# Kernel optimization log

Hardware: AMD Instinct MI355X
Metric: run time of the kernel (lower is better)

The kernel has to match this reference:

```python
import jax, jax.numpy as jnp
import numpy as np

B, I, NN, D = 4, 128, 127, 128   # batch, n_index, nodes without super node, hidden
N = NN + 1                        # nodes including super node
H, L, FFN = 4, 4, 32              # heads, layers, ffn dim
DK = D // H // 2                  # att_size = 16 per head, per stream
SCALE = DK ** -0.5


def layernorm(x, g, b, eps=1e-5):
    m = jnp.mean(x, -1, keepdims=True)
    v = jnp.mean((x - m) ** 2, -1, keepdims=True)
    return (x - m) * jax.lax.rsqrt(v + eps) * g + b


def mha(x, bias, ln_g, ln_b, wq, bq, wk, bk, wv, bv):
    # EncoderLayerSimple: pre-LN then MHA with additive bias, no out-proj (enable_out_layer=False)
    y = layernorm(x, ln_g, ln_b)
    Bx, S, _ = y.shape
    q = (y @ wq.T + bq).reshape(Bx, S, H, DK) * SCALE
    k = (y @ wk.T + bk).reshape(Bx, S, H, DK)
    v = (y @ wv.T + bv).reshape(Bx, S, H, DK)
    s = jnp.einsum('bihd,bjhd->bhij', q, k) + bias
    a = jax.nn.softmax(s, axis=-1)
    return jnp.einsum('bhij,bjhd->bihd', a, v).reshape(Bx, S, H * DK)


def setup_inputs():
    ks = jax.random.split(jax.random.key(0), 24)
    f = jnp.float32
    inp = {
        'node_embedded': jax.random.normal(ks[0], (B, I, NN, D), f),
        'heights': jax.random.normal(ks[1], (B, I, NN, D), f),
        'rel_pos_mat': jax.random.randint(ks[2], (B, I, N, N), 0, 192),
        'tree_attn_bias': jax.random.normal(ks[3], (B, I, N, N), f) * 0.1,
        'index_attn_bias': jax.random.normal(ks[4], (B, N, I, I), f) * 0.1,
        'super_node_emb': jax.random.normal(ks[5], (1, D), f) * 0.02,
        'rel_pos_emb': (jax.random.normal(ks[6], (192, H), f) * 0.02).at[0].set(0.0),  # padding_idx=0
        'super_dist': jax.random.normal(ks[7], (1, H), f) * 0.02,
        'attn_out_w': jax.random.normal(ks[8], (D, D), f) * 0.02,
        'attn_out_b': jnp.zeros((D,), f),
        'ffn_ln_g': jnp.ones((D,), f), 'ffn_ln_b': jnp.zeros((D,), f),
        'ffn_w1': jax.random.normal(ks[9], (FFN, D), f) * 0.02,
        'ffn_b1': jnp.zeros((FFN,), f),
        'ffn_w2': jax.random.normal(ks[10], (D, FFN), f) * 0.02,
        'ffn_b2': jnp.zeros((D,), f),
        'final_ln_g': jnp.ones((D,), f), 'final_ln_b': jnp.zeros((D,), f),
    }
    for pre, base in (('enc1', 11), ('enc2', 17)):
        inp[pre + '_ln_g'] = jnp.ones((L, D), f)
        inp[pre + '_ln_b'] = jnp.zeros((L, D), f)
        for j, nm in enumerate(('wq', 'wk', 'wv')):
            inp[pre + '_' + nm] = jax.random.normal(ks[base + j], (L, H * DK, D), f) * 0.02
            inp[pre + '_b' + nm[1]] = jnp.zeros((L, H * DK), f)
    return inp


def reference(node_embedded, heights, rel_pos_mat, tree_attn_bias, index_attn_bias,
              super_node_emb, rel_pos_emb, super_dist, attn_out_w, attn_out_b,
              ffn_ln_g, ffn_ln_b, ffn_w1, ffn_b1, ffn_w2, ffn_b2, final_ln_g, final_ln_b,
              enc1_ln_g, enc1_ln_b, enc1_wq, enc1_bq, enc1_wk, enc1_bk, enc1_wv, enc1_bv,
              enc2_ln_g, enc2_ln_b, enc2_wq, enc2_bq, enc2_wk, enc2_bk, enc2_wv, enc2_bv):
    node = node_embedded + heights
    sup = jnp.broadcast_to(super_node_emb.reshape(1, 1, 1, D), (B, I, 1, D))
    x = jnp.concatenate([sup, node], axis=2)  # [B, I, N, D]
    # tree attention bias: per-head repeat + rel-pos embedding gather + super-node distance
    rel = rel_pos_emb[rel_pos_mat.reshape(B * I, N, N)]            # [BI, N, N, H]
    tab = tree_attn_bias.reshape(B * I, N, N)[:, None] + jnp.transpose(rel, (0, 3, 1, 2))
    t = super_dist.reshape(1, H, 1)
    tab = tab.at[:, :, 1:, 0].add(t)
    tab = tab.at[:, :, 0, :].add(t)                                # [BI, H, N, N]
    iab = index_attn_bias.reshape(B * N, I, I)[:, None]            # [BN, 1, I, I] (broadcast over heads)
    for l in range(L):
        x1 = jnp.transpose(x, (0, 2, 1, 3)).reshape(B * N, I, D)   # index-axis stream
        x2 = x.reshape(B * I, N, D)                                # node-axis stream
        y1 = mha(x1, iab, enc1_ln_g[l], enc1_ln_b[l], enc1_wq[l], enc1_bq[l],
                 enc1_wk[l], enc1_bk[l], enc1_wv[l], enc1_bv[l])
        y2 = mha(x2, tab, enc2_ln_g[l], enc2_ln_b[l], enc2_wq[l], enc2_bq[l],
                 enc2_wk[l], enc2_bk[l], enc2_wv[l], enc2_bv[l])
        y1 = jnp.transpose(y1.reshape(B, N, I, D // 2), (0, 2, 1, 3))
        y2 = y2.reshape(B, I, N, D // 2)
        y = jnp.concatenate([y1, y2], axis=-1) @ attn_out_w.T + attn_out_b
        x = x + y
        z = layernorm(x, ffn_ln_g, ffn_ln_b)
        z = jax.nn.gelu(z @ ffn_w1.T + ffn_b1, approximate=False) @ ffn_w2.T + ffn_b2
        x = x + z
    return layernorm(x, final_ln_g, final_ln_b)
```

## Files before the change

### kernel.cpp

```cpp
#include <hip/hip_runtime.h>
#include <cstdint>
#include <cstddef>


__device__ __forceinline__ int swz (int r, int c){ return c ^ (((r >> 2) & 7) << 2); }
__device__ __forceinline__ int swzA(int r, int c){ return c ^ ((r & 7) << 2); }

__global__ __launch_bounds__(256) void k_build_x(const float4* __restrict__ ne,
    const float4* __restrict__ hts, const float4* __restrict__ sup,
    float4* __restrict__ X){
  int idx = blockIdx.x * 256 + threadIdx.x;
  int d4 = idx & 31;
  int n  = (idx >> 5) & 127;
  int bi = idx >> 12;
  float4 v;
  if (n == 0){
    v = sup[d4];
  } else {
    size_t s = ((size_t)bi * 127 + (n - 1)) * 32 + d4;
    float4 a = ne[s], h = hts[s];
    v.x = a.x + h.x; v.y = a.y + h.y; v.z = a.z + h.z; v.w = a.w + h.w;
  }
  X[idx] = v;
}

struct QkvArgs {
  const float* x;
  const float* ln_g[2]; const float* ln_b[2];
  const float* w[6];  const float* wb[6];
  float* out[6];
};

__global__ __launch_bounds__(256, 3) void k_qkv(QkvArgs A){
  __shared__ float sY[32 * 128];
  __shared__ float sW[64 * 128];
  const int r0  = blockIdx.x * 32;
  const int enc = blockIdx.y;
  const int t   = threadIdx.x;
  {
    const float4* xs = (const float4*)(A.x + (size_t)r0 * 128);
    #pragma unroll
    for (int it = 0; it < 4; ++it){
      int el = it * 256 + t;
      int rr = el >> 5, c4 = (el & 31) * 4;
      *(float4*)&sY[rr * 128 + swzA(rr, c4)] = xs[el];
    }
  }
  __syncthreads();
  const int row = t >> 3, part = t & 7;
  float s1 = 0.f, s2 = 0.f;
  float4 xv[4];
  #pragma unroll
  for (int q = 0; q < 4; ++q){
    int c4 = part * 16 + q * 4;
    xv[q] = *(const float4*)&sY[row * 128 + swzA(row, c4)];
    s1 += xv[q].x + xv[q].y + xv[q].z + xv[q].w;
    s2 += xv[q].x*xv[q].x + xv[q].y*xv[q].y + xv[q].z*xv[q].z + xv[q].w*xv[q].w;
  }
  s1 += __shfl_xor(s1, 1); s2 += __shfl_xor(s2, 1);
  s1 += __shfl_xor(s1, 2); s2 += __shfl_xor(s2, 2);
  s1 += __shfl_xor(s1, 4); s2 += __shfl_xor(s2, 4);
  float mean = s1 * (1.f / 128.f);
  float rstd = rsqrtf(s2 * (1.f / 128.f) - mean * mean + 1e-5f);
  {
    const float* lg = A.ln_g[enc];
    const float* lb = A.ln_b[enc];
    #pragma unroll
    for (int q = 0; q < 4; ++q){
      int cc = part * 16 + q * 4;
      int a  = row * 128 + swzA(row, cc);
      float4 gv = *(const float4*)&lg[cc];
      float4 bv = *(const float4*)&lb[cc];
      float4 y;
      y.x = (xv[q].x - mean) * rstd * gv.x + bv.x;
      y.y = (xv[q].y - mean) * rstd * gv.y + bv.y;
      y.z = (xv[q].z - mean) * rstd * gv.z + bv.z;
      y.w = (xv[q].w - mean) * rstd * gv.w + bv.w;
      *(float4*)&sY[a] = y;
    }
  }
  const int tc = t & 15, tr = t >> 4;
  const int kb_x  = (tc & 7) << 2;
  const int ra0 = tr * 2, ra1 = tr * 2 + 1;
  const int ka_x0 = (ra0 & 7) << 2;
  const int ka_x1 = (ra1 & 7) << 2;
  for (int g3 = 0; g3 < 3; ++g3){
    const int g = enc * 3 + g3;
    __syncthreads();
    {
      const float4* wsrc = (const float4*)A.w[g];
      #pragma unroll
      for (int it = 0; it < 8; ++it){
        int el = it * 256 + t;
        int rr = el >> 5, c4 = (el & 31) * 4;
        *(float4*)&sW[rr * 128 + swz(rr, c4)] = wsrc[el];
      }
    }
    __syncthreads();
    float acc[2][4] = {};
    #pragma unroll
    for (int k = 0; k < 128; k += 4){
      float4 av[2], bv[4];
      av[0] = *(const float4*)&sY[ra0 * 128 + (k ^ ka_x0)];
      av[1] = *(const float4*)&sY[ra1 * 128 + (k ^ ka_x1)];
      int kb = k ^ kb_x;
      #pragma unroll
      for (int q = 0; q < 4; ++q) bv[q] = *(const float4*)&sW[(tc * 4 + q) * 128 + kb];
      #pragma unroll
      for (int i2 = 0; i2 < 2; ++i2)
        #pragma unroll
        for (int j2 = 0; j2 < 4; ++j2){
          acc[i2][j2] += av[i2].x * bv[j2].x;
          acc[i2][j2] += av[i2].y * bv[j2].y;
          acc[i2][j2] += av[i2].z * bv[j2].z;
          acc[i2][j2] += av[i2].w * bv[j2].w;
        }
    }
    const float scale = (g3 == 0) ? 0.25f : 1.0f;
    const float* wb = A.wb[g];
    const float b0 = wb[tc*4], b1 = wb[tc*4+1], b2 = wb[tc*4+2], b3 = wb[tc*4+3];
    float* outp = A.out[g];
    const int h_ = tc >> 2, u_ = (tc & 3) * 4;
    #pragma unroll
    for (int i2 = 0; i2 < 2; ++i2){
      int gr = r0 + tr * 2 + i2;
      size_t off = ((size_t)((gr >> 7) * 4 + h_)) * 2048 + (gr & 127) * 16 + u_;
      float4 o;
      o.x = (acc[i2][0] + b0) * scale;
      o.y = (acc[i2][1] + b1) * scale;
      o.z = (acc[i2][2] + b2) * scale;
      o.w = (acc[i2][3] + b3) * scale;
      *(float4*)&outp[off] = o;
    }
  }
}

__global__ __launch_bounds__(128, 3) void k_attn1(const float* __restrict__ Q,
    const float* __restrict__ K, const float* __restrict__ V,
    const float* __restrict__ iab, float* __restrict__ YC){
  __shared__ float sK[128][20];
  __shared__ float sV[128][20];
  const int seq = blockIdx.x;
  const int h   = blockIdx.y;
  const int i   = threadIdx.x;
  const int b_ = seq >> 7, n_ = seq & 127;
  const size_t rbase = ((size_t)((b_ * 128 + i) * 4 + h)) * 2048 + n_ * 16;
  #pragma unroll
  for (int u = 0; u < 4; ++u){
    *(float4*)&sK[i][u * 4] = *(const float4*)&K[rbase + u * 4];
    *(float4*)&sV[i][u * 4] = *(const float4*)&V[rbase + u * 4];
  }
  float q[16];
  #pragma unroll
  for (int u = 0; u < 4; ++u){
    float4 v = *(const float4*)&Q[rbase + u * 4];
    q[u*4+0] = v.x; q[u*4+1] = v.y; q[u*4+2] = v.z; q[u*4+3] = v.w;
  }
  __syncthreads();
  const float4* brow = (const float4*)(iab + (size_t)seq * 16384 + (size_t)i * 128);
  float s[128];
  #pragma unroll
  for (int j4 = 0; j4 < 32; ++j4){
    float4 bv4 = brow[j4];
    float bb[4] = {bv4.x, bv4.y, bv4.z, bv4.w};
    #pragma unroll
    for (int u = 0; u < 4; ++u){
      int j = j4 * 4 + u;
      float acc = bb[u];
      #pragma unroll
      for (int u4 = 0; u4 < 4; ++u4){
        float4 kv = *(const float4*)&sK[j][u4 * 4];
        acc += q[u4*4+0]*kv.x + q[u4*4+1]*kv.y + q[u4*4+2]*kv.z + q[u4*4+3]*kv.w;
      }
      s[j] = acc;
    }
  }
  float m = -1e30f;
  #pragma unroll
  for (int j = 0; j < 128; ++j) m = fmaxf(m, s[j]);
  float sum = 0.f;
  #pragma unroll
  for (int j = 0; j < 128; ++j){ float ev = __expf(s[j] - m); s[j] = ev; sum += ev; }
  float inv = 1.f / sum;
  float o[16] = {};
  #pragma unroll
  for (int j = 0; j < 128; ++j){
    float p = s[j];
    #pragma unroll
    for (int u4 = 0; u4 < 4; ++u4){
      float4 vv = *(const float4*)&sV[j][u4 * 4];
      o[u4*4+0] += p * vv.x; o[u4*4+1] += p * vv.y;
      o[u4*4+2] += p * vv.z; o[u4*4+3] += p * vv.w;
    }
  }
  size_t off = (((size_t)(b_ * 128 + i)) * 128 + n_) * 128 + h * 16;
  #pragma unroll
  for (int u = 0; u < 4; ++u){
    float4 v;
    v.x = o[u*4+0]*inv; v.y = o[u*4+1]*inv; v.z = o[u*4+2]*inv; v.w = o[u*4+3]*inv;
    *(float4*)&YC[off + u * 4] = v;
  }
}

__global__ __launch_bounds__(128, 3) void k_attn2(const float* __restrict__ Q,
    const float* __restrict__ K, const float* __restrict__ V,
    const float* __restrict__ tree, const int* __restrict__ mat,
    const float* __restrict__ relemb, const float* __restrict__ sdist,
    float* __restrict__ YC){
  __shared__ float sK[128][20];
  __shared__ float sV[128][20];
  __shared__ float srel[768];
  const int seq = blockIdx.x;
  const int h   = blockIdx.y;
  const int i   = threadIdx.x;
  const size_t base = ((size_t)(seq * 4 + h)) * 2048;
  #pragma unroll
  for (int u = 0; u < 4; ++u){
    *(float4*)&sK[i][u * 4] = *(const float4*)&K[base + i * 16 + u * 4];
    *(float4*)&sV[i][u * 4] = *(const float4*)&V[base + i * 16 + u * 4];
  }
  float q[16];
  #pragma unroll
  for (int u = 0; u < 4; ++u){
    float4 v = *(const float4*)&Q[base + i * 16 + u * 4];
    q[u*4+0] = v.x; q[u*4+1] = v.y; q[u*4+2] = v.z; q[u*4+3] = v.w;
  }
  #pragma unroll
  for (int u = 0; u < 6; ++u) srel[u * 128 + i] = relemb[u * 128 + i];
  const float tsup = sdist[h];
  __syncthreads();
  const float4* trow = (const float4*)(tree + (size_t)seq * 16384 + (size_t)i * 128);
  const int4*   mrow = (const int4*)(mat + (size_t)seq * 16384 + (size_t)i * 128);
  float s[128];
  #pragma unroll
  for (int j4 = 0; j4 < 32; ++j4){
    float4 tv = trow[j4];
    int4  mv  = mrow[j4];
    float bb[4];
    bb[0] = tv.x + srel[mv.x * 4 + h];
    bb[1] = tv.y + srel[mv.y * 4 + h];
    bb[2] = tv.z + srel[mv.z * 4 + h];
    bb[3] = tv.w + srel[mv.w * 4 + h];
    #pragma unroll
    for (int u = 0; u < 4; ++u){
      int j = j4 * 4 + u;
      float acc = bb[u];
      if (i == 0) acc += tsup;
      else if (j == 0) acc += tsup;
      #pragma unroll
      for (int u4 = 0; u4 < 4; ++u4){
        float4 kv = *(const float4*)&sK[j][u4 * 4];
        acc += q[u4*4+0]*kv.x + q[u4*4+1]*kv.y + q[u4*4+2]*kv.z + q[u4*4+3]*kv.w;
      }
      s[j] = acc;
    }
  }
  float m = -1e30f;
  #pragma unroll
  for (int j = 0; j < 128; ++j) m = fmaxf(m, s[j]);
  float sum = 0.f;
  #pragma unroll
  for (int j = 0; j < 128; ++j){ float ev = __expf(s[j] - m); s[j] = ev; sum += ev; }
  float inv = 1.f / sum;
  float o[16] = {};
  #pragma unroll
  for (int j = 0; j < 128; ++j){
    float p = s[j];
    #pragma unroll
    for (int u4 = 0; u4 < 4; ++u4){
      float4 vv = *(const float4*)&sV[j][u4 * 4];
      o[u4*4+0] += p * vv.x; o[u4*4+1] += p * vv.y;
      o[u4*4+2] += p * vv.z; o[u4*4+3] += p * vv.w;
    }
  }
  size_t off = (((size_t)seq) * 128 + i) * 128 + 64 + h * 16;
  #pragma unroll
  for (int u = 0; u < 4; ++u){
    float4 v;
    v.x = o[u*4+0]*inv; v.y = o[u*4+1]*inv; v.z = o[u*4+2]*inv; v.w = o[u*4+3]*inv;
    *(float4*)&YC[off + u * 4] = v;
  }
}

__global__ __launch_bounds__(256, 2) void k_attn_out(const float* __restrict__ YC,
    const float* __restrict__ W, const float* __restrict__ bias, float* __restrict__ X){
  __shared__ float sA[64 * 128];
  __shared__ float sW[64 * 128];
  const int r0 = blockIdx.x * 64, c0 = blockIdx.y * 64;
  const int t  = threadIdx.x;
  {
    const float4* as   = (const float4*)(YC + (size_t)r0 * 128);
    const float4* wsrc = (const float4*)(W + (size_t)c0 * 128);
    #pragma unroll
    for (int it = 0; it < 8; ++it){
      int e  = it * 256 + t;
      int rr = e >> 5, c4 = (e & 31) * 4;
      int cs = swz(rr, c4);
      *(float4*)&sA[rr * 128 + cs] = as[e];
      *(float4*)&sW[rr * 128 + cs] = wsrc[e];
    }
  }
  __syncthreads();
  const int tc = t & 15, tr = t >> 4;
  float acc[4][4] = {};
  #pragma unroll
  for (int k = 0; k < 128; k += 4){
    float4 av[4], bv[4];
    int ka = k ^ ((tr & 7) << 2);
    int kb = k ^ ((tc & 7) << 2);
    #pragma unroll
    for (int q = 0; q < 4; ++q) av[q] = *(const float4*)&sA[(tr * 4 + q) * 128 + ka];
    #pragma unroll
    for (int q = 0; q < 4; ++q) bv[q] = *(const float4*)&sW[(tc * 4 + q) * 128 + kb];
    #pragma unroll
    for (int i2 = 0; i2 < 4; ++i2)
      #pragma unroll
      for (int j2 = 0; j2 < 4; ++j2){
        acc[i2][j2] += av[i2].x * bv[j2].x;
        acc[i2][j2] += av[i2].y * bv[j2].y;
        acc[i2][j2] += av[i2].z * bv[j2].z;
        acc[i2][j2] += av[i2].w * bv[j2].w;
      }
  }
  const float b0 = bias[c0 + tc*4], b1 = bias[c0 + tc*4 + 1],
              b2 = bias[c0 + tc*4 + 2], b3 = bias[c0 + tc*4 + 3];
  #pragma unroll
  for (int i2 = 0; i2 < 4; ++i2){
    int r = r0 + tr * 4 + i2;
    float4* xp = (float4*)&X[(size_t)r * 128 + c0 + tc * 4];
    float4 xv = *xp;
    xv.x += acc[i2][0] + b0;
    xv.y += acc[i2][1] + b1;
    xv.z += acc[i2][2] + b2;
    xv.w += acc[i2][3] + b3;
    *xp = xv;
  }
}

__global__ __launch_bounds__(256, 2) void k_ffn(float* __restrict__ X,
    const float* __restrict__ lg, const float* __restrict__ lb,
    const float* __restrict__ W1, const float* __restrict__ b1,
    const float* __restrict__ W2, const float* __restrict__ b2){
  __shared__ float sW1[32][132];
  __shared__ float sW2[128][36];
  __shared__ float sY[16][132];
  __shared__ float sH[16][33];
  const int t  = threadIdx.x;
  const int r0 = blockIdx.x * 16;
  {
    const float4* w1s = (const float4*)W1;
    #pragma unroll
    for (int it = 0; it < 4; ++it){
      int e = it * 256 + t;
      int r = e >> 5, c4 = (e & 31) * 4;
      *(float4*)&sW1[r][c4] = w1s[e];
    }
    const float4* w2s = (const float4*)W2;
    #pragma unroll
    for (int it = 0; it < 4; ++it){
      int e = it * 256 + t;
      int r = e >> 3, c4 = (e & 7) * 4;
      *(float4*)&sW2[r][c4] = w2s[e];
    }
  }
  const int row = t >> 4, p = t & 15;
  const size_t gb = ((size_t)(r0 + row)) * 128;
  float4 xa = *(const float4*)&X[gb + p * 8];
  float4 xb = *(const float4*)&X[gb + p * 8 + 4];
  float s1 = xa.x + xa.y + xa.z + xa.w + xb.x + xb.y + xb.z + xb.w;
  float s2 = xa.x*xa.x + xa.y*xa.y + xa.z*xa.z + xa.w*xa.w
           + xb.x*xb.x + xb.y*xb.y + xb.z*xb.z + xb.w*xb.w;
  #pragma unroll
  for (int msk = 1; msk < 16; msk <<= 1){ s1 += __shfl_xor(s1, msk); s2 += __shfl_xor(s2, msk); }
  float mean = s1 * (1.f / 128.f);
  float rstd = rsqrtf(s2 * (1.f / 128.f) - mean * mean + 1e-5f);
  {
    float4 g0 = *(const float4*)&lg[p * 8], g1 = *(const float4*)&lg[p * 8 + 4];
    float4 c0 = *(const float4*)&lb[p * 8], c1 = *(const float4*)&lb[p * 8 + 4];
    float4 y0, y1;
    y0.x = (xa.x-mean)*rstd*g0.x + c0.x;  y0.y = (xa.y-mean)*rstd*g0.y + c0.y;
    y0.z = (xa.z-mean)*rstd*g0.z + c0.z;  y0.w = (xa.w-mean)*rstd*g0.w + c0.w;
    y1.x = (xb.x-mean)*rstd*g1.x + c1.x;  y1.y = (xb.y-mean)*rstd*g1.y + c1.y;
    y1.z = (xb.z-mean)*rstd*g1.z + c1.z;  y1.w = (xb.w-mean)*rstd*g1.w + c1.w;
    *(float4*)&sY[row][p * 8]     = y0;
    *(float4*)&sY[row][p * 8 + 4] = y1;
  }
  __syncthreads();
  #pragma unroll
  for (int cc = 0; cc < 2; ++cc){
    int c = p + cc * 16;
    float acc = b1[c];
    #pragma unroll
    for (int k = 0; k < 128; ++k) acc += sY[row][k] * sW1[c][k];
    sH[row][c] = 0.5f * acc * (1.0f + erff(acc * 0.70710678118654752f));
  }
  __syncthreads();
  #pragma unroll
  for (int u = 0; u < 8; ++u){
    int c = p + u * 16;
    float acc = b2[c];
    #pragma unroll
    for (int k = 0; k < 32; ++k) acc += sH[row][k] * sW2[c][k];
    X[gb + c] += acc;
  }
}

__global__ __launch_bounds__(256) void k_final(const float* __restrict__ X,
    const float* __restrict__ g, const float* __restrict__ b, float* __restrict__ out){
  const int t = threadIdx.x;
  const int row = blockIdx.x * 64 + (t >> 2), p = t & 3;
  const float* src = X + (size_t)row * 128 + p * 32;
  float4 v[8];
  float s1 = 0.f, s2 = 0.f;
  #pragma unroll
  for (int u = 0; u < 8; ++u){
    v[u] = *(const float4*)&src[u * 4];
    s1 += v[u].x + v[u].y + v[u].z + v[u].w;
    s2 += v[u].x*v[u].x + v[u].y*v[u].y + v[u].z*v[u].z + v[u].w*v[u].w;
  }
  s1 += __shfl_xor(s1, 1); s2 += __shfl_xor(s2, 1);
  s1 += __shfl_xor(s1, 2); s2 += __shfl_xor(s2, 2);
  float mean = s1 * (1.f / 128.f);
  float rstd = rsqrtf(s2 * (1.f / 128.f) - mean * mean + 1e-5f);
  float* dst = out + (size_t)row * 128 + p * 32;
  #pragma unroll
  for (int u = 0; u < 8; ++u){
    int c = p * 32 + u * 4;
    float4 gv = *(const float4*)&g[c];
    float4 bv = *(const float4*)&b[c];
    float4 o;
    o.x = (v[u].x - mean) * rstd * gv.x + bv.x;
    o.y = (v[u].y - mean) * rstd * gv.y + bv.y;
    o.z = (v[u].z - mean) * rstd * gv.z + bv.z;
    o.w = (v[u].w - mean) * rstd * gv.w + bv.w;
    *(float4*)&dst[u * 4] = o;
  }
}

extern "C" void kernel_launch(void* const* d_in, const int* in_sizes, int n_in,
                              void* d_out, int out_size, void* d_ws, size_t ws_size,
                              hipStream_t stream){
  (void)in_sizes; (void)n_in; (void)out_size; (void)ws_size;
  const float* node_embedded   = (const float*)d_in[0];
  const float* heights         = (const float*)d_in[1];
  const int*   rel_pos_mat     = (const int*)d_in[2];
  const float* tree_attn_bias  = (const float*)d_in[3];
  const float* index_attn_bias = (const float*)d_in[4];
  const float* super_node_emb  = (const float*)d_in[5];
  const float* rel_pos_emb     = (const float*)d_in[6];
  const float* super_dist      = (const float*)d_in[7];
  const float* attn_out_w      = (const float*)d_in[8];
  const float* attn_out_b      = (const float*)d_in[9];
  const float* ffn_ln_g        = (const float*)d_in[10];
  const float* ffn_ln_b        = (const float*)d_in[11];
  const float* ffn_w1          = (const float*)d_in[12];
  const float* ffn_b1          = (const float*)d_in[13];
  const float* ffn_w2          = (const float*)d_in[14];
  const float* ffn_b2          = (const float*)d_in[15];
  const float* final_ln_g      = (const float*)d_in[16];
  const float* final_ln_b      = (const float*)d_in[17];
  const float* e1_ln_g = (const float*)d_in[18];
  const float* e1_ln_b = (const float*)d_in[19];
  const float* e1_wq   = (const float*)d_in[20];
  const float* e1_bq   = (const float*)d_in[21];
  const float* e1_wk   = (const float*)d_in[22];
  const float* e1_bk   = (const float*)d_in[23];
  const float* e1_wv   = (const float*)d_in[24];
  const float* e1_bv   = (const float*)d_in[25];
  const float* e2_ln_g = (const float*)d_in[26];
  const float* e2_ln_b = (const float*)d_in[27];
  const float* e2_wq   = (const float*)d_in[28];
  const float* e2_bq   = (const float*)d_in[29];
  const float* e2_wk   = (const float*)d_in[30];
  const float* e2_bk   = (const float*)d_in[31];
  const float* e2_wv   = (const float*)d_in[32];
  const float* e2_bv   = (const float*)d_in[33];

  float* ws = (float*)d_ws;
  const size_t SZX = 8388608, SZH = 4194304;
  float* X  = ws;
  float* Q1 = X  + SZX;
  float* K1 = Q1 + SZH;
  float* V1 = K1 + SZH;
  float* Q2 = V1 + SZH;
  float* K2 = Q2 + SZH;
  float* V2 = K2 + SZH;
  float* YC = V2 + SZH;

  k_build_x<<<8192, 256, 0, stream>>>((const float4*)node_embedded, (const float4*)heights,
                                      (const float4*)super_node_emb, (float4*)X);
  for (int l = 0; l < 4; ++l){
    QkvArgs A;
    A.x = X;
    A.ln_g[0] = e1_ln_g + l * 128;  A.ln_b[0] = e1_ln_b + l * 128;
    A.ln_g[1] = e2_ln_g + l * 128;  A.ln_b[1] = e2_ln_b + l * 128;
    A.w[0] = e1_wq + (size_t)l * 8192;  A.wb[0] = e1_bq + l * 64;
    A.w[1] = e1_wk + (size_t)l * 8192;  A.wb[1] = e1_bk + l * 64;
    A.w[2] = e1_wv + (size_t)l * 8192;  A.wb[2] = e1_bv + l * 64;
    A.w[3] = e2_wq + (size_t)l * 8192;  A.wb[3] = e2_bq + l * 64;
    A.w[4] = e2_wk + (size_t)l * 8192;  A.wb[4] = e2_bk + l * 64;
    A.w[5] = e2_wv + (size_t)l * 8192;  A.wb[5] = e2_bv + l * 64;
    A.out[0] = Q1; A.out[1] = K1; A.out[2] = V1;
    A.out[3] = Q2; A.out[4] = K2; A.out[5] = V2;
    k_qkv<<<dim3(2048, 2), 256, 0, stream>>>(A);
    k_attn1<<<dim3(512, 4), 128, 0, stream>>>(Q1, K1, V1, index_attn_bias, YC);
    k_attn2<<<dim3(512, 4), 128, 0, stream>>>(Q2, K2, V2, tree_attn_bias, rel_pos_mat,
                                              rel_pos_emb, super_dist, YC);
    k_attn_out<<<dim3(1024, 2), 256, 0, stream>>>(YC, attn_out_w, attn_out_b, X);
    k_ffn<<<4096, 256, 0, stream>>>(X, ffn_ln_g, ffn_ln_b, ffn_w1, ffn_b1, ffn_w2, ffn_b2);
  }
  k_final<<<1024, 256, 0, stream>>>(X, final_ln_g, final_ln_b, (float*)d_out);
}
```

Before: 2.062 ms.

## Split attention key range across four threads per query row

Both attention kernels now use 512 threads per block, with four threads per query row. Each thread handles 32 of the 128 keys, and max, sum and output are combined with xor shuffles. This cuts per-thread register use from a 128-float score array to 32, which should raise occupancy, and K/V shared memory uses an XOR swizzle instead of padding. The cost is extra shuffles for the 16-element output reduction, and every thread still loads the full 16-float query.

```diff
diff --git a/kernel.cpp b/kernel.cpp
--- a/kernel.cpp
+++ b/kernel.cpp
@@ -135,20 +135,21 @@
   }
 }
 
-__global__ __launch_bounds__(128, 3) void k_attn1(const float* __restrict__ Q,
+__global__ __launch_bounds__(512, 4) void k_attn1(const float* __restrict__ Q,
     const float* __restrict__ K, const float* __restrict__ V,
     const float* __restrict__ iab, float* __restrict__ YC){
-  __shared__ float sK[128][20];
-  __shared__ float sV[128][20];
+  __shared__ float sK[128][16];
+  __shared__ float sV[128][16];
   const int seq = blockIdx.x;
   const int h   = blockIdx.y;
-  const int i   = threadIdx.x;
+  const int t   = threadIdx.x;
+  const int i   = t >> 2, qd = t & 3;
   const int b_ = seq >> 7, n_ = seq & 127;
   const size_t rbase = ((size_t)((b_ * 128 + i) * 4 + h)) * 2048 + n_ * 16;
-  #pragma unroll
-  for (int u = 0; u < 4; ++u){
-    *(float4*)&sK[i][u * 4] = *(const float4*)&K[rbase + u * 4];
-    *(float4*)&sV[i][u * 4] = *(const float4*)&V[rbase + u * 4];
+  {
+    int swc = (qd * 4) ^ ((i >> 5) << 2);
+    *(float4*)&sK[i][swc] = *(const float4*)&K[rbase + qd * 4];
+    *(float4*)&sV[i][swc] = *(const float4*)&V[rbase + qd * 4];
   }
   float q[16];
   #pragma unroll
@@ -157,67 +158,77 @@
     q[u*4+0] = v.x; q[u*4+1] = v.y; q[u*4+2] = v.z; q[u*4+3] = v.w;
   }
   __syncthreads();
-  const float4* brow = (const float4*)(iab + (size_t)seq * 16384 + (size_t)i * 128);
-  float s[128];
-  #pragma unroll
-  for (int j4 = 0; j4 < 32; ++j4){
-    float4 bv4 = brow[j4];
+  const float4* brow = (const float4*)(iab + (size_t)seq * 16384 + (size_t)i * 128 + qd * 32);
+  const int jsw = qd << 2;
+  float s[32];
+  #pragma unroll
+  for (int j8 = 0; j8 < 8; ++j8){
+    float4 bv4 = brow[j8];
     float bb[4] = {bv4.x, bv4.y, bv4.z, bv4.w};
     #pragma unroll
     for (int u = 0; u < 4; ++u){
-      int j = j4 * 4 + u;
+      int jj = j8 * 4 + u;
+      int j  = qd * 32 + jj;
       float acc = bb[u];
       #pragma unroll
       for (int u4 = 0; u4 < 4; ++u4){
-        float4 kv = *(const float4*)&sK[j][u4 * 4];
+        float4 kv = *(const float4*)&sK[j][(u4 * 4) ^ jsw];
         acc += q[u4*4+0]*kv.x + q[u4*4+1]*kv.y + q[u4*4+2]*kv.z + q[u4*4+3]*kv.w;
       }
-      s[j] = acc;
+      s[jj] = acc;
     }
   }
   float m = -1e30f;
   #pragma unroll
-  for (int j = 0; j < 128; ++j) m = fmaxf(m, s[j]);
+  for (int jj = 0; jj < 32; ++jj) m = fmaxf(m, s[jj]);
+  m = fmaxf(m, __shfl_xor(m, 1));
+  m = fmaxf(m, __shfl_xor(m, 2));
   float sum = 0.f;
   #pragma unroll
-  for (int j = 0; j < 128; ++j){ float ev = __expf(s[j] - m); s[j] = ev; sum += ev; }
+  for (int jj = 0; jj < 32; ++jj){ float ev = __expf(s[jj] - m); s[jj] = ev; sum += ev; }
+  sum += __shfl_xor(sum, 1);
+  sum += __shfl_xor(sum, 2);
   float inv = 1.f / sum;
   float o[16] = {};
   #pragma unroll
-  for (int j = 0; j < 128; ++j){
-    float p = s[j];
+  for (int jj = 0; jj < 32; ++jj){
+    int j = qd * 32 + jj;
+    float p = s[jj];
     #pragma unroll
     for (int u4 = 0; u4 < 4; ++u4){
-      float4 vv = *(const float4*)&sV[j][u4 * 4];
+      float4 vv = *(const float4*)&sV[j][(u4 * 4) ^ jsw];
       o[u4*4+0] += p * vv.x; o[u4*4+1] += p * vv.y;
       o[u4*4+2] += p * vv.z; o[u4*4+3] += p * vv.w;
     }
   }
-  size_t off = (((size_t)(b_ * 128 + i)) * 128 + n_) * 128 + h * 16;
-  #pragma unroll
-  for (int u = 0; u < 4; ++u){
-    float4 v;
-    v.x = o[u*4+0]*inv; v.y = o[u*4+1]*inv; v.z = o[u*4+2]*inv; v.w = o[u*4+3]*inv;
-    *(float4*)&YC[off + u * 4] = v;
-  }
-}
-
-__global__ __launch_bounds__(128, 3) void k_attn2(const float* __restrict__ Q,
+  #pragma unroll
+  for (int e = 0; e < 16; ++e){
+    o[e] += __shfl_xor(o[e], 1);
+    o[e] += __shfl_xor(o[e], 2);
+  }
+  size_t off = (((size_t)(b_ * 128 + i)) * 128 + n_) * 128 + h * 16 + qd * 4;
+  float4 v;
+  v.x = o[qd*4+0]*inv; v.y = o[qd*4+1]*inv; v.z = o[qd*4+2]*inv; v.w = o[qd*4+3]*inv;
+  *(float4*)&YC[off] = v;
+}
+
+__global__ __launch_bounds__(512, 4) void k_attn2(const float* __restrict__ Q,
     const float* __restrict__ K, const float* __restrict__ V,
     const float* __restrict__ tree, const int* __restrict__ mat,
     const float* __restrict__ relemb, const float* __restrict__ sdist,
     float* __restrict__ YC){
-  __shared__ float sK[128][20];
-  __shared__ float sV[128][20];
+  __shared__ float sK[128][16];
+  __shared__ float sV[128][16];
   __shared__ float srel[768];
   const int seq = blockIdx.x;
   const int h   = blockIdx.y;
-  const int i   = threadIdx.x;
+  const int t   = threadIdx.x;
+  const int i   = t >> 2, qd = t & 3;
   const size_t base = ((size_t)(seq * 4 + h)) * 2048;
-  #pragma unroll
-  for (int u = 0; u < 4; ++u){
-    *(float4*)&sK[i][u * 4] = *(const float4*)&K[base + i * 16 + u * 4];
-    *(float4*)&sV[i][u * 4] = *(const float4*)&V[base + i * 16 + u * 4];
+  {
+    int swc = (qd * 4) ^ ((i >> 5) << 2);
+    *(float4*)&sK[i][swc] = *(const float4*)&K[base + i * 16 + qd * 4];
+    *(float4*)&sV[i][swc] = *(const float4*)&V[base + i * 16 + qd * 4];
   }
   float q[16];
   #pragma unroll
@@ -225,17 +236,17 @@
     float4 v = *(const float4*)&Q[base + i * 16 + u * 4];
     q[u*4+0] = v.x; q[u*4+1] = v.y; q[u*4+2] = v.z; q[u*4+3] = v.w;
   }
-  #pragma unroll
-  for (int u = 0; u < 6; ++u) srel[u * 128 + i] = relemb[u * 128 + i];
+  for (int u = t; u < 768; u += 512) srel[u] = relemb[u];
   const float tsup = sdist[h];
   __syncthreads();
-  const float4* trow = (const float4*)(tree + (size_t)seq * 16384 + (size_t)i * 128);
-  const int4*   mrow = (const int4*)(mat + (size_t)seq * 16384 + (size_t)i * 128);
-  float s[128];
-  #pragma unroll
-  for (int j4 = 0; j4 < 32; ++j4){
-    float4 tv = trow[j4];
-    int4  mv  = mrow[j4];
+  const float4* trow = (const float4*)(tree + (size_t)seq * 16384 + (size_t)i * 128 + qd * 32);
+  const int4*   mrow = (const int4*)(mat + (size_t)seq * 16384 + (size_t)i * 128 + qd * 32);
+  const int jsw = qd << 2;
+  float s[32];
+  #pragma unroll
+  for (int j8 = 0; j8 < 8; ++j8){
+    float4 tv = trow[j8];
+    int4  mv  = mrow[j8];
     float bb[4];
     bb[0] = tv.x + srel[mv.x * 4 + h];
     bb[1] = tv.y + srel[mv.y * 4 + h];
@@ -243,43 +254,51 @@
     bb[3] = tv.w + srel[mv.w * 4 + h];
     #pragma unroll
     for (int u = 0; u < 4; ++u){
-      int j = j4 * 4 + u;
+      int jj = j8 * 4 + u;
+      int j  = qd * 32 + jj;
       float acc = bb[u];
       if (i == 0) acc += tsup;
       else if (j == 0) acc += tsup;
       #pragma unroll
       for (int u4 = 0; u4 < 4; ++u4){
-        float4 kv = *(const float4*)&sK[j][u4 * 4];
+        float4 kv = *(const float4*)&sK[j][(u4 * 4) ^ jsw];
         acc += q[u4*4+0]*kv.x + q[u4*4+1]*kv.y + q[u4*4+2]*kv.z + q[u4*4+3]*kv.w;
       }
-      s[j] = acc;
+      s[jj] = acc;
     }
   }
   float m = -1e30f;
   #pragma unroll
-  for (int j = 0; j < 128; ++j) m = fmaxf(m, s[j]);
+  for (int jj = 0; jj < 32; ++jj) m = fmaxf(m, s[jj]);
+  m = fmaxf(m, __shfl_xor(m, 1));
+  m = fmaxf(m, __shfl_xor(m, 2));
   float sum = 0.f;
   #pragma unroll
-  for (int j = 0; j < 128; ++j){ float ev = __expf(s[j] - m); s[j] = ev; sum += ev; }
+  for (int jj = 0; jj < 32; ++jj){ float ev = __expf(s[jj] - m); s[jj] = ev; sum += ev; }
+  sum += __shfl_xor(sum, 1);
+  sum += __shfl_xor(sum, 2);
   float inv = 1.f / sum;
   float o[16] = {};
   #pragma unroll
-  for (int j = 0; j < 128; ++j){
-    float p = s[j];
+  for (int jj = 0; jj < 32; ++jj){
+    int j = qd * 32 + jj;
+    float p = s[jj];
     #pragma unroll
     for (int u4 = 0; u4 < 4; ++u4){
-      float4 vv = *(const float4*)&sV[j][u4 * 4];
+      float4 vv = *(const float4*)&sV[j][(u4 * 4) ^ jsw];
       o[u4*4+0] += p * vv.x; o[u4*4+1] += p * vv.y;
       o[u4*4+2] += p * vv.z; o[u4*4+3] += p * vv.w;
     }
   }
-  size_t off = (((size_t)seq) * 128 + i) * 128 + 64 + h * 16;
-  #pragma unroll
-  for (int u = 0; u < 4; ++u){
-    float4 v;
-    v.x = o[u*4+0]*inv; v.y = o[u*4+1]*inv; v.z = o[u*4+2]*inv; v.w = o[u*4+3]*inv;
-    *(float4*)&YC[off + u * 4] = v;
-  }
+  #pragma unroll
+  for (int e = 0; e < 16; ++e){
+    o[e] += __shfl_xor(o[e], 1);
+    o[e] += __shfl_xor(o[e], 2);
+  }
+  size_t off = (((size_t)seq) * 128 + i) * 128 + 64 + h * 16 + qd * 4;
+  float4 v;
+  v.x = o[qd*4+0]*inv; v.y = o[qd*4+1]*inv; v.z = o[qd*4+2]*inv; v.w = o[qd*4+3]*inv;
+  *(float4*)&YC[off] = v;
 }
 
 __global__ __launch_bounds__(256, 2) void k_attn_out(const float* __restrict__ YC,
@@ -503,8 +522,8 @@
     A.out[0] = Q1; A.out[1] = K1; A.out[2] = V1;
     A.out[3] = Q2; A.out[4] = K2; A.out[5] = V2;
     k_qkv<<<dim3(2048, 2), 256, 0, stream>>>(A);
-    k_attn1<<<dim3(512, 4), 128, 0, stream>>>(Q1, K1, V1, index_attn_bias, YC);
-    k_attn2<<<dim3(512, 4), 128, 0, stream>>>(Q2, K2, V2, tree_attn_bias, rel_pos_mat,
+    k_attn1<<<dim3(512, 4), 512, 0, stream>>>(Q1, K1, V1, index_attn_bias, YC);
+    k_attn2<<<dim3(512, 4), 512, 0, stream>>>(Q2, K2, V2, tree_attn_bias, rel_pos_mat,
                                               rel_pos_emb, super_dist, YC);
     k_attn_out<<<dim3(1024, 2), 256, 0, stream>>>(YC, attn_out_w, attn_out_b, X);
     k_ffn<<<4096, 256, 0, stream>>>(X, ffn_ln_g, ffn_ln_b, ffn_w1, ffn_b1, ffn_w2, ffn_b2);
```

New measurement: 2.131 ms. +3.4%, slower.
